# Performance work log

Measured on AMD Instinct MI355X. Metric: run time of the kernel, lower is better.

The kernel has to match this reference:

```python
import jax, jax.numpy as jnp
import numpy as np

B, T, D = 8, 1024, 1024

def setup_inputs() -> dict:
    key = jax.random.key(0)
    ks = jax.random.split(key, 9)
    s = D ** -0.5
    return {
        "x": jax.random.normal(ks[0], (B, T, D), dtype=jnp.float32),
        "w_q": jax.random.normal(ks[1], (D, D), dtype=jnp.float32) * s,
        "b_q": jax.random.normal(ks[2], (D,), dtype=jnp.float32) * 0.02,
        "w_k": jax.random.normal(ks[3], (D, D), dtype=jnp.float32) * s,
        "b_k": jax.random.normal(ks[4], (D,), dtype=jnp.float32) * 0.02,
        "w_v": jax.random.normal(ks[5], (D, D), dtype=jnp.float32) * s,
        "b_v": jax.random.normal(ks[6], (D,), dtype=jnp.float32) * 0.02,
        "w_o": jax.random.normal(ks[7], (D, D), dtype=jnp.float32) * s,
        "b_o": jax.random.normal(ks[8], (D,), dtype=jnp.float32) * 0.02,
    }

def reference(x, w_q, b_q, w_k, b_k, w_v, b_v, w_o, b_o):
    d = x.shape[-1]
    scale = jnp.asarray(d, x.dtype) ** -0.5
    q = jnp.einsum('btd,ed->bte', x, w_q) + b_q  # nn.Linear: x @ W^T + b
    k = jnp.einsum('btd,ed->bte', x, w_k) + b_k
    v = jnp.einsum('btd,ed->bte', x, w_v) + b_v
    t = x.shape[1]
    causal = jnp.tril(jnp.ones((t, t), dtype=bool))  # (T, T)
    scores = jnp.einsum('bqd,bkd->bqk', q, k) * scale
    scores = jnp.where(causal, scores, -jnp.inf)
    attn = jax.nn.softmax(scores, axis=-1)  # max-subtraction folded in
    out = jnp.einsum('bqk,bkd->bqd', attn, v)
    return jnp.einsum('btd,ed->bte', out, w_o) + b_o
```

## Files before the change

### kernel.cpp

```cpp
#include <hip/hip_runtime.h>

typedef unsigned short u16;
typedef __attribute__((ext_vector_type(8))) short short8;
typedef __attribute__((ext_vector_type(4))) float f32x4;


__device__ __forceinline__ u16 f2bf(float f) {
  unsigned u = __builtin_bit_cast(unsigned, f);
  u += 0x7fffu + ((u >> 16) & 1u);
  return (u16)(u >> 16);
}

__device__ __forceinline__ void gload16(const void* g, void* l) {
  __builtin_amdgcn_global_load_lds(
      (const __attribute__((address_space(1))) unsigned*)g,
      (__attribute__((address_space(3))) unsigned*)l, 16, 0, 0);
}

__device__ __forceinline__ void gemm_tile(
    const u16* __restrict__ A, int lda,
    const u16* __restrict__ B, int ldb,
    int m0, int n0, int kend,
    char* sA, char* sB, f32x4 acc[4][4])
{
  const int tid  = threadIdx.x;
  const int lane = tid & 63;
  const int wave = tid >> 6;
  const int quad = lane >> 4;
  const int l16  = lane & 15;
  const int wr   = (wave >> 1) << 6;
  const int wc   = (wave & 1) << 6;

  const u16* ga[4]; const u16* gb[4]; int lb[4];
#pragma unroll
  for (int j = 0; j < 4; ++j) {
    const int Lb = j * 256 + wave * 64;
    const int L  = Lb + lane;
    const int r  = L >> 3;
    const int c  = (L & 7) ^ (r & 7);
    lb[j] = Lb * 16;
    ga[j] = A + (size_t)(m0 + r) * lda + c * 8;
    gb[j] = B + (size_t)(n0 + r) * ldb + c * 8;
  }

  for (int kt = 0; kt < kend; kt += 64) {
#pragma unroll
    for (int j = 0; j < 4; ++j) {
      gload16(ga[j], sA + lb[j]);
      gload16(gb[j], sB + lb[j]);
      ga[j] += 64; gb[j] += 64;
    }
    __syncthreads();
#pragma unroll
    for (int kk = 0; kk < 2; ++kk) {
      short8 af[4], bfr[4];
#pragma unroll
      for (int i = 0; i < 4; ++i) {
        const int rm = wr + i * 16 + l16;
        af[i]  = *(const short8*)(sA + rm * 128 + (((kk << 2) + quad) ^ (rm & 7)) * 16);
        const int rn = wc + i * 16 + l16;
        bfr[i] = *(const short8*)(sB + rn * 128 + (((kk << 2) + quad) ^ (rn & 7)) * 16);
      }
#pragma unroll
      for (int i = 0; i < 4; ++i)
#pragma unroll
        for (int j = 0; j < 4; ++j)
          acc[i][j] = __builtin_amdgcn_mfma_f32_16x16x32_bf16(af[i], bfr[j], acc[i][j], 0, 0, 0);
    }
    __syncthreads();
  }
}

#define ACC_ZERO(acc) { const f32x4 z4 = {0.f,0.f,0.f,0.f}; \
  _Pragma("unroll") for (int i=0;i<4;++i) _Pragma("unroll") for (int j=0;j<4;++j) acc[i][j]=z4; }

__device__ __forceinline__ void store_tile_bf16(
    f32x4 acc[4][4], const float* bias, int nbias0,
    u16* C, int m0, int n0, int ldc, char* smem)
{
  const int tid = threadIdx.x, lane = tid & 63, wave = tid >> 6;
  const int quad = lane >> 4, l16 = lane & 15;
  const int wr = (wave >> 1) << 6, wc = (wave & 1) << 6;
  u16* t = (u16*)smem;
#pragma unroll
  for (int j = 0; j < 4; ++j) {
    const int nn = wc + j * 16 + l16;
    const float bj = bias ? bias[nbias0 + nn] : 0.f;
#pragma unroll
    for (int i = 0; i < 4; ++i) {
      const int mm = wr + i * 16 + quad * 4;
#pragma unroll
      for (int r = 0; r < 4; ++r)
        t[(mm + r) * 136 + nn] = f2bf(acc[i][j][r] + bj);
    }
  }
  __syncthreads();
#pragma unroll
  for (int it = 0; it < 8; ++it) {
    const int L = it * 256 + tid;
    const int mm = L >> 4, cc = L & 15;
    *(uint4*)(C + (size_t)(m0 + mm) * ldc + n0 + cc * 8) =
        *(const uint4*)(t + mm * 136 + cc * 8);
  }
}

__global__ __launch_bounds__(256) void cast_inputs(
    const float* __restrict__ x,  const float* __restrict__ wq,
    const float* __restrict__ wk, const float* __restrict__ wv,
    const float* __restrict__ wo,
    u16* xb, u16* wqb, u16* wkb, u16* wvb, u16* wob)
{
  int b = blockIdx.x;
  const float* src; u16* dst; int base;
  if (b < 4096) { src = x; dst = xb; base = b * 2048; }
  else {
    int r = (b - 4096) >> 9, bb = (b - 4096) & 511;
    base = bb * 2048;
    src = (r == 0) ? wq : (r == 1) ? wk : (r == 2) ? wv : wo;
    dst = (r == 0) ? wqb : (r == 1) ? wkb : (r == 2) ? wvb : wob;
  }
  int i0 = base + threadIdx.x * 8;
  float4 f0 = *(const float4*)(src + i0);
  float4 f1 = *(const float4*)(src + i0 + 4);
  short8 o;
  o[0]=(short)f2bf(f0.x); o[1]=(short)f2bf(f0.y); o[2]=(short)f2bf(f0.z); o[3]=(short)f2bf(f0.w);
  o[4]=(short)f2bf(f1.x); o[5]=(short)f2bf(f1.y); o[6]=(short)f2bf(f1.z); o[7]=(short)f2bf(f1.w);
  *(short8*)(dst + i0) = o;
}

__global__ __launch_bounds__(256) void proj_qkv(
    const u16* __restrict__ xb,
    const u16* __restrict__ wqb, const u16* __restrict__ wkb, const u16* __restrict__ wvb,
    const float* __restrict__ bq, const float* __restrict__ bk, const float* __restrict__ bv,
    u16* q, u16* k, u16* vt)
{
  __shared__ char smem[34816];
  char* sA = smem; char* sB = smem + 16384;
  const int z = blockIdx.z;
  const u16* W = (z == 0) ? wqb : (z == 1) ? wkb : wvb;
  const float* bias = (z == 0) ? bq : (z == 1) ? bk : bv;
  const int id = blockIdx.x + 8 * blockIdx.y;
  const int m0 = ((id & 7) * 8 + (id >> 6)) * 128;
  const int n0 = ((id >> 3) & 7) * 128;

  f32x4 acc[4][4]; ACC_ZERO(acc);
  gemm_tile(xb, 1024, W, 1024, m0, n0, 1024, sA, sB, acc);

  if (z < 2) {
    store_tile_bf16(acc, bias, n0, (z == 0) ? q : k, m0, n0, 1024, smem);
  } else {
    const int tid = threadIdx.x, lane = tid & 63, wave = tid >> 6;
    const int quad = lane >> 4, l16 = lane & 15;
    const int wr = (wave >> 1) << 6, wc = (wave & 1) << 6;
    u16* t = (u16*)smem;
#pragma unroll
    for (int j = 0; j < 4; ++j) {
      const int nn = wc + j * 16 + l16;
      const float bj = bias[n0 + nn];
#pragma unroll
      for (int i = 0; i < 4; ++i) {
        const int mm = wr + i * 16 + quad * 4;
#pragma unroll
        for (int r = 0; r < 4; ++r)
          t[nn * 136 + mm + r] = f2bf(acc[i][j][r] + bj);
      }
    }
    __syncthreads();
    const int b = m0 >> 10, t0 = m0 & 1023;
#pragma unroll
    for (int it = 0; it < 8; ++it) {
      const int L = it * 256 + tid;
      const int nn = L >> 4, cc = L & 15;
      *(uint4*)(vt + ((size_t)b << 20) + (size_t)(n0 + nn) * 1024 + t0 + cc * 8) =
          *(const uint4*)(t + nn * 136 + cc * 8);
    }
  }
}

__global__ __launch_bounds__(256) void qk_expscores(
    const u16* __restrict__ q, const u16* __restrict__ k,
    u16* __restrict__ probs, float* __restrict__ rowsum)
{
  const int id = blockIdx.x;
  const int b = id / 36, t = id - b * 36;
  const int qb = (t >= 28) ? 7 : (t >= 21) ? 6 : (t >= 15) ? 5 : (t >= 10) ? 4
               : (t >= 6) ? 3 : (t >= 3) ? 2 : (t >= 1) ? 1 : 0;
  const int kb = t - qb * (qb + 1) / 2;

  __shared__ char smem[34816];
  const u16* A = q + ((size_t)b << 20);
  const u16* B = k + ((size_t)b << 20);
  const int m0 = qb * 128, n0 = kb * 128;

  f32x4 acc[4][4]; ACC_ZERO(acc);
  gemm_tile(A, 1024, B, 1024, m0, n0, 1024, smem, smem + 16384, acc);

  const int tid = threadIdx.x, lane = tid & 63, wave = tid >> 6;
  const int quad = lane >> 4, l16 = lane & 15;
  const int wr = (wave >> 1) << 6, wc = (wave & 1) << 6;
  const bool diag = (kb == qb);

  float part[4][4];
#pragma unroll
  for (int i = 0; i < 4; ++i)
#pragma unroll
    for (int r = 0; r < 4; ++r) part[i][r] = 0.f;

  u16* tl = (u16*)smem;
#pragma unroll
  for (int j = 0; j < 4; ++j) {
    const int nn = wc + j * 16 + l16;
#pragma unroll
    for (int i = 0; i < 4; ++i) {
      const int mm = wr + i * 16 + quad * 4;
#pragma unroll
      for (int r = 0; r < 4; ++r) {
        float e = __expf(acc[i][j][r] * 0.03125f);
        if (diag && nn > mm + r) e = 0.f;
        part[i][r] += e;
        tl[(mm + r) * 136 + nn] = f2bf(e);
      }
    }
  }
  float* rs = rowsum + b * 1024 + m0;
#pragma unroll
  for (int i = 0; i < 4; ++i)
#pragma unroll
    for (int r = 0; r < 4; ++r) {
      float v = part[i][r];
      v += __shfl_xor(v, 1); v += __shfl_xor(v, 2);
      v += __shfl_xor(v, 4); v += __shfl_xor(v, 8);
      if (l16 == 0) atomicAdd(rs + wr + i * 16 + quad * 4 + r, v);
    }
  __syncthreads();
  u16* C = probs + ((size_t)b << 20);
#pragma unroll
  for (int it = 0; it < 8; ++it) {
    const int L = it * 256 + tid;
    const int mm = L >> 4, cc = L & 15;
    *(uint4*)(C + (size_t)(m0 + mm) * 1024 + n0 + cc * 8) =
        *(const uint4*)(tl + mm * 136 + cc * 8);
  }
}

__global__ __launch_bounds__(256) void pv_gemm(
    const u16* __restrict__ probs, const u16* __restrict__ vt,
    const float* __restrict__ rowsum, u16* __restrict__ o)
{
  const int id = blockIdx.x;
  const int b = id & 7, nb = (id >> 3) & 7, qb = 7 - (id >> 6);
  __shared__ char smem[34816];
  const u16* A = probs + ((size_t)b << 20);
  const u16* B = vt + ((size_t)b << 20);
  const int m0 = qb * 128, n0 = nb * 128;
  const int kend = (qb + 1) * 128;

  f32x4 acc[4][4]; ACC_ZERO(acc);
  gemm_tile(A, 1024, B, 1024, m0, n0, kend, smem, smem + 16384, acc);

  const int tid = threadIdx.x, lane = tid & 63, wave = tid >> 6;
  const int quad = lane >> 4, l16 = lane & 15;
  const int wr = (wave >> 1) << 6, wc = (wave & 1) << 6;
  const float* rs = rowsum + b * 1024 + m0;
  u16* tl = (u16*)smem;
#pragma unroll
  for (int i = 0; i < 4; ++i)
#pragma unroll
    for (int r = 0; r < 4; ++r) {
      const int mm = wr + i * 16 + quad * 4 + r;
      const float inv = 1.0f / rs[mm];
#pragma unroll
      for (int j = 0; j < 4; ++j)
        tl[mm * 136 + wc + j * 16 + l16] = f2bf(acc[i][j][r] * inv);
    }
  __syncthreads();
  u16* C = o + ((size_t)b << 20);
#pragma unroll
  for (int it = 0; it < 8; ++it) {
    const int L = it * 256 + tid;
    const int mm = L >> 4, cc = L & 15;
    *(uint4*)(C + (size_t)(m0 + mm) * 1024 + n0 + cc * 8) =
        *(const uint4*)(tl + mm * 136 + cc * 8);
  }
}

__global__ __launch_bounds__(256) void proj_o(
    const u16* __restrict__ ob, const u16* __restrict__ wob,
    const float* __restrict__ bo, float* __restrict__ out)
{
  __shared__ char smem[34816];
  const int id = blockIdx.x;
  const int m0 = ((id & 7) * 8 + (id >> 6)) * 128;
  const int n0 = ((id >> 3) & 7) * 128;
  f32x4 acc[4][4]; ACC_ZERO(acc);
  gemm_tile(ob, 1024, wob, 1024, m0, n0, 1024, smem, smem + 16384, acc);

  const int tid = threadIdx.x, lane = tid & 63, wave = tid >> 6;
  const int quad = lane >> 4, l16 = lane & 15;
  const int wr = (wave >> 1) << 6, wc = (wave & 1) << 6;
  float* tf = (float*)smem;
#pragma unroll
  for (int half = 0; half < 2; ++half) {
    if (wr == half * 64) {
#pragma unroll
      for (int j = 0; j < 4; ++j) {
        const int nn = wc + j * 16 + l16;
        const float bj = bo[n0 + nn];
#pragma unroll
        for (int i = 0; i < 4; ++i)
#pragma unroll
          for (int r = 0; r < 4; ++r)
            tf[(i * 16 + quad * 4 + r) * 132 + nn] = acc[i][j][r] + bj;
      }
    }
    __syncthreads();
#pragma unroll
    for (int it = 0; it < 8; ++it) {
      const int L = it * 256 + tid;
      const int mm = L >> 5, cc = L & 31;
      *(float4*)(out + (size_t)(m0 + half * 64 + mm) * 1024 + n0 + cc * 4) =
          *(const float4*)(tf + mm * 132 + cc * 4);
    }
    __syncthreads();
  }
}

extern "C" void kernel_launch(void* const* d_in, const int* in_sizes, int n_in,
                              void* d_out, int out_size, void* d_ws, size_t ws_size,
                              hipStream_t stream) {
  const float* x  = (const float*)d_in[0];
  const float* wq = (const float*)d_in[1];
  const float* bq = (const float*)d_in[2];
  const float* wk = (const float*)d_in[3];
  const float* bk = (const float*)d_in[4];
  const float* wv = (const float*)d_in[5];
  const float* bv = (const float*)d_in[6];
  const float* wo = (const float*)d_in[7];
  const float* bo = (const float*)d_in[8];
  float* out = (float*)d_out;

  char* ws = (char*)d_ws;
  const size_t MB = 1u << 20;
  u16*  xb  = (u16*)(ws);
  u16*  wqb = (u16*)(ws + 16*MB);
  u16*  wkb = (u16*)(ws + 18*MB);
  u16*  wvb = (u16*)(ws + 20*MB);
  u16*  wob = (u16*)(ws + 22*MB);
  u16*  qb  = (u16*)(ws + 24*MB);
  u16*  kb  = (u16*)(ws + 40*MB);
  u16*  vtb = (u16*)(ws + 56*MB);
  u16*  pr  = (u16*)(ws + 72*MB);
  float* rsum = (float*)(ws + 88*MB);

  cast_inputs<<<6144, 256, 0, stream>>>(x, wq, wk, wv, wo, xb, wqb, wkb, wvb, wob);
  hipMemsetAsync(rsum, 0, 8192 * sizeof(float), stream);
  proj_qkv<<<dim3(8, 64, 3), 256, 0, stream>>>(xb, wqb, wkb, wvb, bq, bk, bv, qb, kb, vtb);
  qk_expscores<<<288, 256, 0, stream>>>(qb, kb, pr, rsum);
  pv_gemm<<<512, 256, 0, stream>>>(pr, vtb, rsum, xb );
  proj_o<<<512, 256, 0, stream>>>(xb, wob, bo, out);
}
```

Before: 236.3 us.

## Switch GEMM tiles to 32x32x16 MFMA and fold rowsum zeroing into cast kernel

Replaces the 4x4 grid of 16x16x32 bf16 MFMAs per wave with a 2x2 grid of 32x32x16 MFMAs. This halves the LDS fragment loads per k-step and uses the larger, more throughput-efficient matrix instruction. All epilogues are remapped to the 32x32 accumulator row layout. Separately, the hipMemsetAsync of the rowsum buffer is removed and the first 8 blocks of the cast kernel zero it instead, saving one launch. The risk is an error in the new accumulator-to-row index mapping.

```diff
diff --git a/kernel.cpp b/kernel.cpp
--- a/kernel.cpp
+++ b/kernel.cpp
@@ -2,7 +2,7 @@
 
 typedef unsigned short u16;
 typedef __attribute__((ext_vector_type(8))) short short8;
-typedef __attribute__((ext_vector_type(4))) float f32x4;
+typedef __attribute__((ext_vector_type(16))) float f32x16;
 
 
 __device__ __forceinline__ u16 f2bf(float f) {
@@ -21,13 +21,13 @@
     const u16* __restrict__ A, int lda,
     const u16* __restrict__ B, int ldb,
     int m0, int n0, int kend,
-    char* sA, char* sB, f32x4 acc[4][4])
+    char* sA, char* sB, f32x16 acc[2][2])
 {
   const int tid  = threadIdx.x;
   const int lane = tid & 63;
   const int wave = tid >> 6;
-  const int quad = lane >> 4;
-  const int l16  = lane & 15;
+  const int r32  = lane & 31;
+  const int halfl = lane >> 5;
   const int wr   = (wave >> 1) << 6;
   const int wc   = (wave & 1) << 6;
 
@@ -43,6 +43,9 @@
     gb[j] = B + (size_t)(n0 + r) * ldb + c * 8;
   }
 
+  const int rmA0 = wr + r32, rmA1 = wr + 32 + r32;
+  const int rnB0 = wc + r32, rnB1 = wc + 32 + r32;
+
   for (int kt = 0; kt < kend; kt += 64) {
 #pragma unroll
     for (int j = 0; j < 4; ++j) {
@@ -52,47 +55,44 @@
     }
     __syncthreads();
 #pragma unroll
-    for (int kk = 0; kk < 2; ++kk) {
-      short8 af[4], bfr[4];
-#pragma unroll
-      for (int i = 0; i < 4; ++i) {
-        const int rm = wr + i * 16 + l16;
-        af[i]  = *(const short8*)(sA + rm * 128 + (((kk << 2) + quad) ^ (rm & 7)) * 16);
-        const int rn = wc + i * 16 + l16;
-        bfr[i] = *(const short8*)(sB + rn * 128 + (((kk << 2) + quad) ^ (rn & 7)) * 16);
-      }
-#pragma unroll
-      for (int i = 0; i < 4; ++i)
-#pragma unroll
-        for (int j = 0; j < 4; ++j)
-          acc[i][j] = __builtin_amdgcn_mfma_f32_16x16x32_bf16(af[i], bfr[j], acc[i][j], 0, 0, 0);
-    }
-    __syncthreads();
-  }
-}
-
-#define ACC_ZERO(acc) { const f32x4 z4 = {0.f,0.f,0.f,0.f}; \
-  _Pragma("unroll") for (int i=0;i<4;++i) _Pragma("unroll") for (int j=0;j<4;++j) acc[i][j]=z4; }
+    for (int ks = 0; ks < 4; ++ks) {
+      const int ch = ks * 2 + halfl;
+      short8 a0 = *(const short8*)(sA + rmA0 * 128 + ((ch ^ (rmA0 & 7)) * 16));
+      short8 a1 = *(const short8*)(sA + rmA1 * 128 + ((ch ^ (rmA1 & 7)) * 16));
+      short8 b0 = *(const short8*)(sB + rnB0 * 128 + ((ch ^ (rnB0 & 7)) * 16));
+      short8 b1 = *(const short8*)(sB + rnB1 * 128 + ((ch ^ (rnB1 & 7)) * 16));
+      acc[0][0] = __builtin_amdgcn_mfma_f32_32x32x16_bf16(a0, b0, acc[0][0], 0, 0, 0);
+      acc[0][1] = __builtin_amdgcn_mfma_f32_32x32x16_bf16(a0, b1, acc[0][1], 0, 0, 0);
+      acc[1][0] = __builtin_amdgcn_mfma_f32_32x32x16_bf16(a1, b0, acc[1][0], 0, 0, 0);
+      acc[1][1] = __builtin_amdgcn_mfma_f32_32x32x16_bf16(a1, b1, acc[1][1], 0, 0, 0);
+    }
+    __syncthreads();
+  }
+}
+
+#define ACC_ZERO(acc) { _Pragma("unroll") for (int i=0;i<2;++i) \
+  _Pragma("unroll") for (int j=0;j<2;++j) \
+  _Pragma("unroll") for (int r=0;r<16;++r) acc[i][j][r]=0.f; }
+
+#define CROW(reg, halfl) (((reg) & 3) + 8 * ((reg) >> 2) + 4 * (halfl))
 
 __device__ __forceinline__ void store_tile_bf16(
-    f32x4 acc[4][4], const float* bias, int nbias0,
+    f32x16 acc[2][2], const float* bias, int nbias0,
     u16* C, int m0, int n0, int ldc, char* smem)
 {
   const int tid = threadIdx.x, lane = tid & 63, wave = tid >> 6;
-  const int quad = lane >> 4, l16 = lane & 15;
+  const int r32 = lane & 31, halfl = lane >> 5;
   const int wr = (wave >> 1) << 6, wc = (wave & 1) << 6;
   u16* t = (u16*)smem;
 #pragma unroll
-  for (int j = 0; j < 4; ++j) {
-    const int nn = wc + j * 16 + l16;
+  for (int wj = 0; wj < 2; ++wj) {
+    const int nn = wc + wj * 32 + r32;
     const float bj = bias ? bias[nbias0 + nn] : 0.f;
 #pragma unroll
-    for (int i = 0; i < 4; ++i) {
-      const int mm = wr + i * 16 + quad * 4;
-#pragma unroll
-      for (int r = 0; r < 4; ++r)
-        t[(mm + r) * 136 + nn] = f2bf(acc[i][j][r] + bj);
-    }
+    for (int wi = 0; wi < 2; ++wi)
+#pragma unroll
+      for (int reg = 0; reg < 16; ++reg)
+        t[(wr + wi * 32 + CROW(reg, halfl)) * 136 + nn] = f2bf(acc[wi][wj][reg] + bj);
   }
   __syncthreads();
 #pragma unroll
@@ -108,9 +108,13 @@
     const float* __restrict__ x,  const float* __restrict__ wq,
     const float* __restrict__ wk, const float* __restrict__ wv,
     const float* __restrict__ wo,
-    u16* xb, u16* wqb, u16* wkb, u16* wvb, u16* wob)
+    u16* xb, u16* wqb, u16* wkb, u16* wvb, u16* wob, float* rsum)
 {
   int b = blockIdx.x;
+  if (b < 8) {
+    float4 z = {0.f, 0.f, 0.f, 0.f};
+    *(float4*)(rsum + (b * 256 + threadIdx.x) * 4) = z;
+  }
   const float* src; u16* dst; int base;
   if (b < 4096) { src = x; dst = xb; base = b * 2048; }
   else {
@@ -143,27 +147,25 @@
   const int m0 = ((id & 7) * 8 + (id >> 6)) * 128;
   const int n0 = ((id >> 3) & 7) * 128;
 
-  f32x4 acc[4][4]; ACC_ZERO(acc);
+  f32x16 acc[2][2]; ACC_ZERO(acc);
   gemm_tile(xb, 1024, W, 1024, m0, n0, 1024, sA, sB, acc);
 
   if (z < 2) {
     store_tile_bf16(acc, bias, n0, (z == 0) ? q : k, m0, n0, 1024, smem);
   } else {
     const int tid = threadIdx.x, lane = tid & 63, wave = tid >> 6;
-    const int quad = lane >> 4, l16 = lane & 15;
+    const int r32 = lane & 31, halfl = lane >> 5;
     const int wr = (wave >> 1) << 6, wc = (wave & 1) << 6;
     u16* t = (u16*)smem;
 #pragma unroll
-    for (int j = 0; j < 4; ++j) {
-      const int nn = wc + j * 16 + l16;
+    for (int wj = 0; wj < 2; ++wj) {
+      const int nn = wc + wj * 32 + r32;
       const float bj = bias[n0 + nn];
 #pragma unroll
-      for (int i = 0; i < 4; ++i) {
-        const int mm = wr + i * 16 + quad * 4;
-#pragma unroll
-        for (int r = 0; r < 4; ++r)
-          t[nn * 136 + mm + r] = f2bf(acc[i][j][r] + bj);
-      }
+      for (int wi = 0; wi < 2; ++wi)
+#pragma unroll
+        for (int reg = 0; reg < 16; ++reg)
+          t[nn * 136 + wr + wi * 32 + CROW(reg, halfl)] = f2bf(acc[wi][wj][reg] + bj);
     }
     __syncthreads();
     const int b = m0 >> 10, t0 = m0 & 1023;
@@ -192,45 +194,44 @@
   const u16* B = k + ((size_t)b << 20);
   const int m0 = qb * 128, n0 = kb * 128;
 
-  f32x4 acc[4][4]; ACC_ZERO(acc);
+  f32x16 acc[2][2]; ACC_ZERO(acc);
   gemm_tile(A, 1024, B, 1024, m0, n0, 1024, smem, smem + 16384, acc);
 
   const int tid = threadIdx.x, lane = tid & 63, wave = tid >> 6;
-  const int quad = lane >> 4, l16 = lane & 15;
+  const int r32 = lane & 31, halfl = lane >> 5;
   const int wr = (wave >> 1) << 6, wc = (wave & 1) << 6;
   const bool diag = (kb == qb);
 
-  float part[4][4];
-#pragma unroll
-  for (int i = 0; i < 4; ++i)
-#pragma unroll
-    for (int r = 0; r < 4; ++r) part[i][r] = 0.f;
-
   u16* tl = (u16*)smem;
-#pragma unroll
-  for (int j = 0; j < 4; ++j) {
-    const int nn = wc + j * 16 + l16;
-#pragma unroll
-    for (int i = 0; i < 4; ++i) {
-      const int mm = wr + i * 16 + quad * 4;
-#pragma unroll
-      for (int r = 0; r < 4; ++r) {
-        float e = __expf(acc[i][j][r] * 0.03125f);
-        if (diag && nn > mm + r) e = 0.f;
-        part[i][r] += e;
-        tl[(mm + r) * 136 + nn] = f2bf(e);
+  float part[2][16];
+#pragma unroll
+  for (int wi = 0; wi < 2; ++wi)
+#pragma unroll
+    for (int reg = 0; reg < 16; ++reg) part[wi][reg] = 0.f;
+
+#pragma unroll
+  for (int wj = 0; wj < 2; ++wj) {
+    const int nn = wc + wj * 32 + r32;
+#pragma unroll
+    for (int wi = 0; wi < 2; ++wi)
+#pragma unroll
+      for (int reg = 0; reg < 16; ++reg) {
+        const int mm = wr + wi * 32 + CROW(reg, halfl);
+        float e = __expf(acc[wi][wj][reg] * 0.03125f);
+        if (diag && nn > mm) e = 0.f;
+        part[wi][reg] += e;
+        tl[mm * 136 + nn] = f2bf(e);
       }
-    }
   }
   float* rs = rowsum + b * 1024 + m0;
 #pragma unroll
-  for (int i = 0; i < 4; ++i)
-#pragma unroll
-    for (int r = 0; r < 4; ++r) {
-      float v = part[i][r];
-      v += __shfl_xor(v, 1); v += __shfl_xor(v, 2);
-      v += __shfl_xor(v, 4); v += __shfl_xor(v, 8);
-      if (l16 == 0) atomicAdd(rs + wr + i * 16 + quad * 4 + r, v);
+  for (int wi = 0; wi < 2; ++wi)
+#pragma unroll
+    for (int reg = 0; reg < 16; ++reg) {
+      float v = part[wi][reg];
+      v += __shfl_xor(v, 1);  v += __shfl_xor(v, 2);  v += __shfl_xor(v, 4);
+      v += __shfl_xor(v, 8);  v += __shfl_xor(v, 16);
+      if (r32 == 0) atomicAdd(rs + wr + wi * 32 + CROW(reg, halfl), v);
     }
   __syncthreads();
   u16* C = probs + ((size_t)b << 20);
@@ -255,23 +256,23 @@
   const int m0 = qb * 128, n0 = nb * 128;
   const int kend = (qb + 1) * 128;
 
-  f32x4 acc[4][4]; ACC_ZERO(acc);
+  f32x16 acc[2][2]; ACC_ZERO(acc);
   gemm_tile(A, 1024, B, 1024, m0, n0, kend, smem, smem + 16384, acc);
 
   const int tid = threadIdx.x, lane = tid & 63, wave = tid >> 6;
-  const int quad = lane >> 4, l16 = lane & 15;
+  const int r32 = lane & 31, halfl = lane >> 5;
   const int wr = (wave >> 1) << 6, wc = (wave & 1) << 6;
   const float* rs = rowsum + b * 1024 + m0;
   u16* tl = (u16*)smem;
 #pragma unroll
-  for (int i = 0; i < 4; ++i)
-#pragma unroll
-    for (int r = 0; r < 4; ++r) {
-      const int mm = wr + i * 16 + quad * 4 + r;
+  for (int wi = 0; wi < 2; ++wi)
+#pragma unroll
+    for (int reg = 0; reg < 16; ++reg) {
+      const int mm = wr + wi * 32 + CROW(reg, halfl);
       const float inv = 1.0f / rs[mm];
 #pragma unroll
-      for (int j = 0; j < 4; ++j)
-        tl[mm * 136 + wc + j * 16 + l16] = f2bf(acc[i][j][r] * inv);
+      for (int wj = 0; wj < 2; ++wj)
+        tl[mm * 136 + wc + wj * 32 + r32] = f2bf(acc[wi][wj][reg] * inv);
     }
   __syncthreads();
   u16* C = o + ((size_t)b << 20);
@@ -292,25 +293,25 @@
   const int id = blockIdx.x;
   const int m0 = ((id & 7) * 8 + (id >> 6)) * 128;
   const int n0 = ((id >> 3) & 7) * 128;
-  f32x4 acc[4][4]; ACC_ZERO(acc);
+  f32x16 acc[2][2]; ACC_ZERO(acc);
   gemm_tile(ob, 1024, wob, 1024, m0, n0, 1024, smem, smem + 16384, acc);
 
   const int tid = threadIdx.x, lane = tid & 63, wave = tid >> 6;
-  const int quad = lane >> 4, l16 = lane & 15;
+  const int r32 = lane & 31, halfl = lane >> 5;
   const int wr = (wave >> 1) << 6, wc = (wave & 1) << 6;
   float* tf = (float*)smem;
 #pragma unroll
   for (int half = 0; half < 2; ++half) {
-    if (wr == half * 64) {
-#pragma unroll
-      for (int j = 0; j < 4; ++j) {
-        const int nn = wc + j * 16 + l16;
+    if ((wr >> 6) == half) {
+#pragma unroll
+      for (int wj = 0; wj < 2; ++wj) {
+        const int nn = wc + wj * 32 + r32;
         const float bj = bo[n0 + nn];
 #pragma unroll
-        for (int i = 0; i < 4; ++i)
-#pragma unroll
-          for (int r = 0; r < 4; ++r)
-            tf[(i * 16 + quad * 4 + r) * 132 + nn] = acc[i][j][r] + bj;
+        for (int wi = 0; wi < 2; ++wi)
+#pragma unroll
+          for (int reg = 0; reg < 16; ++reg)
+            tf[(wi * 32 + CROW(reg, halfl)) * 132 + nn] = acc[wi][wj][reg] + bj;
       }
     }
     __syncthreads();
@@ -352,8 +353,7 @@
   u16*  pr  = (u16*)(ws + 72*MB);
   float* rsum = (float*)(ws + 88*MB);
 
-  cast_inputs<<<6144, 256, 0, stream>>>(x, wq, wk, wv, wo, xb, wqb, wkb, wvb, wob);
-  hipMemsetAsync(rsum, 0, 8192 * sizeof(float), stream);
+  cast_inputs<<<6144, 256, 0, stream>>>(x, wq, wk, wv, wo, xb, wqb, wkb, wvb, wob, rsum);
   proj_qkv<<<dim3(8, 64, 3), 256, 0, stream>>>(xb, wqb, wkb, wvb, bq, bk, bv, qb, kb, vtb);
   qk_expscores<<<288, 256, 0, stream>>>(qb, kb, pr, rsum);
   pv_gemm<<<512, 256, 0, stream>>>(pr, vtb, rsum, xb );
```

After: 242.7 us. 2.7% more time.

## Use 64-row tiles for attention and output GEMMs, fold memset into cast kernel

Applied to the files above, without the earlier changes.

Adds a 64x128 GEMM tile variant and uses it in qk_expscores, pv_gemm and proj_o, doubling the grid sizes (576, 1024, 1024 blocks) so the 256 CUs are better filled. The causal triangle is reindexed with a sqrt-based mapping for 64-row query tiles, which also skips more masked work in the PV stage. The rowsum zeroing moves from a separate memset into the cast kernel, removing one launch. The smaller tiles lower data reuse per block and increase the number of K/V tile reloads.

```diff
diff --git a/kernel.cpp b/kernel.cpp
--- a/kernel.cpp
+++ b/kernel.cpp
@@ -71,8 +71,76 @@
   }
 }
 
-#define ACC_ZERO(acc) { const f32x4 z4 = {0.f,0.f,0.f,0.f}; \
-  _Pragma("unroll") for (int i=0;i<4;++i) _Pragma("unroll") for (int j=0;j<4;++j) acc[i][j]=z4; }
+__device__ __forceinline__ void gemm_tile_64(
+    const u16* __restrict__ A, int lda,
+    const u16* __restrict__ B, int ldb,
+    int m0, int n0, int kend,
+    char* sA, char* sB, f32x4 acc[2][4])
+{
+  const int tid  = threadIdx.x;
+  const int lane = tid & 63;
+  const int wave = tid >> 6;
+  const int quad = lane >> 4;
+  const int l16  = lane & 15;
+  const int wr   = (wave >> 1) << 5;
+  const int wc   = (wave & 1) << 6;
+
+  const u16* ga[2]; int la[2];
+  const u16* gb[4]; int lb[4];
+#pragma unroll
+  for (int j = 0; j < 2; ++j) {
+    const int Lb = j * 256 + wave * 64;
+    const int L  = Lb + lane;
+    const int r  = L >> 3;
+    const int c  = (L & 7) ^ (r & 7);
+    la[j] = Lb * 16;
+    ga[j] = A + (size_t)(m0 + r) * lda + c * 8;
+  }
+#pragma unroll
+  for (int j = 0; j < 4; ++j) {
+    const int Lb = j * 256 + wave * 64;
+    const int L  = Lb + lane;
+    const int r  = L >> 3;
+    const int c  = (L & 7) ^ (r & 7);
+    lb[j] = Lb * 16;
+    gb[j] = B + (size_t)(n0 + r) * ldb + c * 8;
+  }
+
+  for (int kt = 0; kt < kend; kt += 64) {
+#pragma unroll
+    for (int j = 0; j < 2; ++j) { gload16(ga[j], sA + la[j]); ga[j] += 64; }
+#pragma unroll
+    for (int j = 0; j < 4; ++j) { gload16(gb[j], sB + lb[j]); gb[j] += 64; }
+    __syncthreads();
+#pragma unroll
+    for (int kk = 0; kk < 2; ++kk) {
+      short8 af[2], bfr[4];
+#pragma unroll
+      for (int i = 0; i < 2; ++i) {
+        const int rm = wr + i * 16 + l16;
+        af[i] = *(const short8*)(sA + rm * 128 + (((kk << 2) + quad) ^ (rm & 7)) * 16);
+      }
+#pragma unroll
+      for (int j = 0; j < 4; ++j) {
+        const int rn = wc + j * 16 + l16;
+        bfr[j] = *(const short8*)(sB + rn * 128 + (((kk << 2) + quad) ^ (rn & 7)) * 16);
+      }
+#pragma unroll
+      for (int i = 0; i < 2; ++i)
+#pragma unroll
+        for (int j = 0; j < 4; ++j)
+          acc[i][j] = __builtin_amdgcn_mfma_f32_16x16x32_bf16(af[i], bfr[j], acc[i][j], 0, 0, 0);
+    }
+    __syncthreads();
+  }
+}
+
+#define ACC_ZERO4(acc) { _Pragma("unroll") for (int i=0;i<4;++i) \
+  _Pragma("unroll") for (int j=0;j<4;++j) \
+  _Pragma("unroll") for (int r=0;r<4;++r) acc[i][j][r]=0.f; }
+#define ACC_ZERO2(acc) { _Pragma("unroll") for (int i=0;i<2;++i) \
+  _Pragma("unroll") for (int j=0;j<4;++j) \
+  _Pragma("unroll") for (int r=0;r<4;++r) acc[i][j][r]=0.f; }
 
 __device__ __forceinline__ void store_tile_bf16(
     f32x4 acc[4][4], const float* bias, int nbias0,
@@ -108,9 +176,13 @@
     const float* __restrict__ x,  const float* __restrict__ wq,
     const float* __restrict__ wk, const float* __restrict__ wv,
     const float* __restrict__ wo,
-    u16* xb, u16* wqb, u16* wkb, u16* wvb, u16* wob)
+    u16* xb, u16* wqb, u16* wkb, u16* wvb, u16* wob, float* rsum)
 {
   int b = blockIdx.x;
+  if (b < 8) {
+    float4 z = {0.f, 0.f, 0.f, 0.f};
+    *(float4*)(rsum + (b * 256 + threadIdx.x) * 4) = z;
+  }
   const float* src; u16* dst; int base;
   if (b < 4096) { src = x; dst = xb; base = b * 2048; }
   else {
@@ -143,7 +215,7 @@
   const int m0 = ((id & 7) * 8 + (id >> 6)) * 128;
   const int n0 = ((id >> 3) & 7) * 128;
 
-  f32x4 acc[4][4]; ACC_ZERO(acc);
+  f32x4 acc[4][4]; ACC_ZERO4(acc);
   gemm_tile(xb, 1024, W, 1024, m0, n0, 1024, sA, sB, acc);
 
   if (z < 2) {
@@ -182,27 +254,31 @@
     u16* __restrict__ probs, float* __restrict__ rowsum)
 {
   const int id = blockIdx.x;
-  const int b = id / 36, t = id - b * 36;
-  const int qb = (t >= 28) ? 7 : (t >= 21) ? 6 : (t >= 15) ? 5 : (t >= 10) ? 4
-               : (t >= 6) ? 3 : (t >= 3) ? 2 : (t >= 1) ? 1 : 0;
-  const int kb = t - qb * (qb + 1) / 2;
-
-  __shared__ char smem[34816];
+  const int b = id / 72, t = id - b * 72;
+  int p = (int)((__builtin_sqrtf((float)(4 * t + 1)) - 1.f) * 0.5f);
+  while ((p + 1) * (p + 2) <= t) ++p;
+  while (p * (p + 1) > t) --p;
+  int r0 = t - p * (p + 1);
+  const int qi = 2 * p + (r0 >= p + 1);
+  const int kb = (r0 >= p + 1) ? r0 - (p + 1) : r0;
+
+  __shared__ char smem[24576];
+  char* sA = smem; char* sB = smem + 8192;
   const u16* A = q + ((size_t)b << 20);
   const u16* B = k + ((size_t)b << 20);
-  const int m0 = qb * 128, n0 = kb * 128;
-
-  f32x4 acc[4][4]; ACC_ZERO(acc);
-  gemm_tile(A, 1024, B, 1024, m0, n0, 1024, smem, smem + 16384, acc);
+  const int m0 = qi * 64, n0 = kb * 128;
+
+  f32x4 acc[2][4]; ACC_ZERO2(acc);
+  gemm_tile_64(A, 1024, B, 1024, m0, n0, 1024, sA, sB, acc);
 
   const int tid = threadIdx.x, lane = tid & 63, wave = tid >> 6;
   const int quad = lane >> 4, l16 = lane & 15;
-  const int wr = (wave >> 1) << 6, wc = (wave & 1) << 6;
-  const bool diag = (kb == qb);
-
-  float part[4][4];
-#pragma unroll
-  for (int i = 0; i < 4; ++i)
+  const int wr = (wave >> 1) << 5, wc = (wave & 1) << 6;
+  const bool diag = (kb == (qi >> 1));
+
+  float part[2][4];
+#pragma unroll
+  for (int i = 0; i < 2; ++i)
 #pragma unroll
     for (int r = 0; r < 4; ++r) part[i][r] = 0.f;
 
@@ -211,12 +287,12 @@
   for (int j = 0; j < 4; ++j) {
     const int nn = wc + j * 16 + l16;
 #pragma unroll
-    for (int i = 0; i < 4; ++i) {
+    for (int i = 0; i < 2; ++i) {
       const int mm = wr + i * 16 + quad * 4;
 #pragma unroll
       for (int r = 0; r < 4; ++r) {
         float e = __expf(acc[i][j][r] * 0.03125f);
-        if (diag && nn > mm + r) e = 0.f;
+        if (diag && (n0 + nn) > (m0 + mm + r)) e = 0.f;
         part[i][r] += e;
         tl[(mm + r) * 136 + nn] = f2bf(e);
       }
@@ -224,7 +300,7 @@
   }
   float* rs = rowsum + b * 1024 + m0;
 #pragma unroll
-  for (int i = 0; i < 4; ++i)
+  for (int i = 0; i < 2; ++i)
 #pragma unroll
     for (int r = 0; r < 4; ++r) {
       float v = part[i][r];
@@ -235,7 +311,7 @@
   __syncthreads();
   u16* C = probs + ((size_t)b << 20);
 #pragma unroll
-  for (int it = 0; it < 8; ++it) {
+  for (int it = 0; it < 4; ++it) {
     const int L = it * 256 + tid;
     const int mm = L >> 4, cc = L & 15;
     *(uint4*)(C + (size_t)(m0 + mm) * 1024 + n0 + cc * 8) =
@@ -248,23 +324,24 @@
     const float* __restrict__ rowsum, u16* __restrict__ o)
 {
   const int id = blockIdx.x;
-  const int b = id & 7, nb = (id >> 3) & 7, qb = 7 - (id >> 6);
-  __shared__ char smem[34816];
+  const int b = id & 7, nb = (id >> 3) & 7, qi = 15 - (id >> 6);
+  __shared__ char smem[24576];
+  char* sA = smem; char* sB = smem + 8192;
   const u16* A = probs + ((size_t)b << 20);
   const u16* B = vt + ((size_t)b << 20);
-  const int m0 = qb * 128, n0 = nb * 128;
-  const int kend = (qb + 1) * 128;
-
-  f32x4 acc[4][4]; ACC_ZERO(acc);
-  gemm_tile(A, 1024, B, 1024, m0, n0, kend, smem, smem + 16384, acc);
+  const int m0 = qi * 64, n0 = nb * 128;
+  const int kend = (qi + 1) * 64;
+
+  f32x4 acc[2][4]; ACC_ZERO2(acc);
+  gemm_tile_64(A, 1024, B, 1024, m0, n0, kend, sA, sB, acc);
 
   const int tid = threadIdx.x, lane = tid & 63, wave = tid >> 6;
   const int quad = lane >> 4, l16 = lane & 15;
-  const int wr = (wave >> 1) << 6, wc = (wave & 1) << 6;
+  const int wr = (wave >> 1) << 5, wc = (wave & 1) << 6;
   const float* rs = rowsum + b * 1024 + m0;
   u16* tl = (u16*)smem;
 #pragma unroll
-  for (int i = 0; i < 4; ++i)
+  for (int i = 0; i < 2; ++i)
 #pragma unroll
     for (int r = 0; r < 4; ++r) {
       const int mm = wr + i * 16 + quad * 4 + r;
@@ -276,7 +353,7 @@
   __syncthreads();
   u16* C = o + ((size_t)b << 20);
 #pragma unroll
-  for (int it = 0; it < 8; ++it) {
+  for (int it = 0; it < 4; ++it) {
     const int L = it * 256 + tid;
     const int mm = L >> 4, cc = L & 15;
     *(uint4*)(C + (size_t)(m0 + mm) * 1024 + n0 + cc * 8) =
@@ -289,39 +366,34 @@
     const float* __restrict__ bo, float* __restrict__ out)
 {
   __shared__ char smem[34816];
+  char* sA = smem; char* sB = smem + 8192;
   const int id = blockIdx.x;
-  const int m0 = ((id & 7) * 8 + (id >> 6)) * 128;
+  const int m0 = ((id & 7) * 16 + (id >> 6)) * 64;
   const int n0 = ((id >> 3) & 7) * 128;
-  f32x4 acc[4][4]; ACC_ZERO(acc);
-  gemm_tile(ob, 1024, wob, 1024, m0, n0, 1024, smem, smem + 16384, acc);
+  f32x4 acc[2][4]; ACC_ZERO2(acc);
+  gemm_tile_64(ob, 1024, wob, 1024, m0, n0, 1024, sA, sB, acc);
 
   const int tid = threadIdx.x, lane = tid & 63, wave = tid >> 6;
   const int quad = lane >> 4, l16 = lane & 15;
-  const int wr = (wave >> 1) << 6, wc = (wave & 1) << 6;
+  const int wr = (wave >> 1) << 5, wc = (wave & 1) << 6;
   float* tf = (float*)smem;
 #pragma unroll
-  for (int half = 0; half < 2; ++half) {
-    if (wr == half * 64) {
-#pragma unroll
-      for (int j = 0; j < 4; ++j) {
-        const int nn = wc + j * 16 + l16;
-        const float bj = bo[n0 + nn];
-#pragma unroll
-        for (int i = 0; i < 4; ++i)
-#pragma unroll
-          for (int r = 0; r < 4; ++r)
-            tf[(i * 16 + quad * 4 + r) * 132 + nn] = acc[i][j][r] + bj;
-      }
-    }
-    __syncthreads();
-#pragma unroll
-    for (int it = 0; it < 8; ++it) {
-      const int L = it * 256 + tid;
-      const int mm = L >> 5, cc = L & 31;
-      *(float4*)(out + (size_t)(m0 + half * 64 + mm) * 1024 + n0 + cc * 4) =
-          *(const float4*)(tf + mm * 132 + cc * 4);
-    }
-    __syncthreads();
+  for (int j = 0; j < 4; ++j) {
+    const int nn = wc + j * 16 + l16;
+    const float bj = bo[n0 + nn];
+#pragma unroll
+    for (int i = 0; i < 2; ++i)
+#pragma unroll
+      for (int r = 0; r < 4; ++r)
+        tf[(wr + i * 16 + quad * 4 + r) * 132 + nn] = acc[i][j][r] + bj;
+  }
+  __syncthreads();
+#pragma unroll
+  for (int it = 0; it < 8; ++it) {
+    const int L = it * 256 + tid;
+    const int mm = L >> 5, cc = L & 31;
+    *(float4*)(out + (size_t)(m0 + mm) * 1024 + n0 + cc * 4) =
+        *(const float4*)(tf + mm * 132 + cc * 4);
   }
 }
 
@@ -352,10 +424,9 @@
   u16*  pr  = (u16*)(ws + 72*MB);
   float* rsum = (float*)(ws + 88*MB);
 
-  cast_inputs<<<6144, 256, 0, stream>>>(x, wq, wk, wv, wo, xb, wqb, wkb, wvb, wob);
-  hipMemsetAsync(rsum, 0, 8192 * sizeof(float), stream);
+  cast_inputs<<<6144, 256, 0, stream>>>(x, wq, wk, wv, wo, xb, wqb, wkb, wvb, wob, rsum);
   proj_qkv<<<dim3(8, 64, 3), 256, 0, stream>>>(xb, wqb, wkb, wvb, bq, bk, bv, qb, kb, vtb);
-  qk_expscores<<<288, 256, 0, stream>>>(qb, kb, pr, rsum);
-  pv_gemm<<<512, 256, 0, stream>>>(pr, vtb, rsum, xb );
-  proj_o<<<512, 256, 0, stream>>>(xb, wob, bo, out);
-}
+  qk_expscores<<<576, 256, 0, stream>>>(qb, kb, pr, rsum);
+  pv_gemm<<<1024, 256, 0, stream>>>(pr, vtb, rsum, xb );
+  proj_o<<<1024, 256, 0, stream>>>(xb, wob, bo, out);
+}
```

After: 225.8 us. 1.05x faster.
